# Kernel tuning notes

Hardware: AMD Instinct MI355X
Metric: run time of the kernel (lower is better)

The kernel has to match this reference:

```python
import jax, jax.numpy as jnp
import numpy as np
from jax import lax

N = 5000
C = 81  # num_classes including background at index 0
BG_OFFSET = 1


def _iou_matrix(b):
    # b: [N,4] as x1,y1,x2,y2 -> pairwise IoU [N,N]
    x1, y1, x2, y2 = b[:, 0], b[:, 1], b[:, 2], b[:, 3]
    area = (x2 - x1) * (y2 - y1)  # [N]
    ix1 = jnp.maximum(x1[:, None], x1[None, :])
    iy1 = jnp.maximum(y1[:, None], y1[None, :])
    ix2 = jnp.minimum(x2[:, None], x2[None, :])
    iy2 = jnp.minimum(y2[:, None], y2[None, :])
    iw = jnp.maximum(ix2 - ix1, 0.0)
    ih = jnp.maximum(iy2 - iy1, 0.0)
    inter = iw * ih
    return inter / (area[:, None] + area[None, :] - inter)


def setup_inputs() -> dict:
    key = jax.random.key(0)
    k1, k2, k3 = jax.random.split(key, 3)
    # valid boxes: x1<x2, y1<y2 on a ~1024px canvas, size ~up to 256px
    xy1 = jax.random.uniform(k1, (N, 2), dtype=jnp.float32) * 1024.0
    wh = jax.random.uniform(k2, (N, 2), dtype=jnp.float32) * 256.0 + 1.0
    bboxes = jnp.concatenate([xy1, xy1 + wh], axis=1)  # [N,4]
    scores = jax.random.uniform(k3, (N, C), dtype=jnp.float32)  # [N,C]
    return {
        "bboxes": bboxes,
        "scores": scores,
        "conf_thresh": 0.6,
        "nms_thresh": 0.5,
        "max_instances": 300,
    }


def _multiclass_nms(bboxes, scores, conf_thresh, nms_thresh, max_instances):
    n = bboxes.shape[0]
    neg_inf = jnp.finfo(scores.dtype).min
    iou = _iou_matrix(bboxes)  # [N,N]

    def nms_one_class(score_c):  # score_c: [N]
        valid = score_c > conf_thresh
        masked = jnp.where(valid, score_c, neg_inf)
        order = jnp.argsort(masked)[::-1]  # descending score

        def step(suppressed, idx):
            keep = valid[idx] & ~suppressed[idx]
            new_sup = jnp.where(keep, suppressed | (iou[idx] > nms_thresh), suppressed)
            return new_sup, keep

        _, keeps = lax.scan(step, jnp.zeros((n,), bool), order)
        # scatter keep flags back to original box order
        return jnp.zeros((n,), bool).at[order].set(keeps)

    fg_scores = scores[:, BG_OFFSET:].T  # [C-1, N]
    keep = jax.vmap(nms_one_class)(fg_scores)  # [C-1, N]

    # global top-k over all (class, box) kept detections, sorted by score desc
    flat = jnp.where(keep, fg_scores, neg_inf).reshape(-1)  # [(C-1)*N]
    top_scores, top_idx = lax.top_k(flat, max_instances)
    cls = top_idx // n + BG_OFFSET  # [K]
    box = top_idx % n  # [K]
    valid_out = top_scores > neg_inf / 2

    sel_score = scores[box, cls]  # differentiable gather
    preds = jnp.concatenate([bboxes[box], sel_score[:, None]], axis=1)  # [K,5]
    preds = jnp.where(valid_out[:, None], preds, 0.0)
    labels = jnp.where(valid_out, cls, -1)
    return preds, labels


def reference(bboxes, scores, conf_thresh, nms_thresh, max_instances):
    return _multiclass_nms(bboxes, scores, conf_thresh, nms_thresh, max_instances)
```

## Files before the change

### kernel.cpp

```cpp
#include <hip/hip_runtime.h>

typedef unsigned long long u64;
typedef unsigned int u32;
typedef unsigned short u16;

#define MSORT 4096
#define TPB1  1024
#define TPBF  1024
#define BOXCAP 3648
#define RSLOT_W 10
#define KPC   300
#define SELCAP 1024
#define PREFR 64

#define WG_SCOPE __HIP_MEMORY_SCOPE_WORKGROUP

__device__ __forceinline__ float boxArea(float4 b) {
    return __fmul_rn(__fsub_rn(b.z, b.x), __fsub_rn(b.w, b.y));
}

template<bool GE>
__device__ __forceinline__ bool iou_gt(float4 a, float area_a, float4 b, float area_b, double B) {
    float ix1 = fmaxf(a.x, b.x), iy1 = fmaxf(a.y, b.y);
    float ix2 = fminf(a.z, b.z), iy2 = fminf(a.w, b.w);
    float iw  = fmaxf(__fsub_rn(ix2, ix1), 0.0f);
    float ih  = fmaxf(__fsub_rn(iy2, iy1), 0.0f);
    float inter = __fmul_rn(iw, ih);
    float uni   = __fsub_rn(__fadd_rn(area_a, area_b), inter);
    return GE ? ((double)inter >= B * (double)uni) : ((double)inter > B * (double)uni);
}

__device__ __forceinline__ int scoreBin(u32 bits) {
    int b = (int)(bits >> 12) - 0x3F000;
    return b < 0 ? 0 : (b > 2047 ? 2047 : b);
}

template<bool GE>
__device__ __forceinline__ int prefix_nms_w0(
    const float* __restrict__ bboxes, const u64* __restrict__ keybuf,
    int R, double B, int tid, int c, int N, u64* __restrict__ gkept_c)
{
    u64 key = (tid < R) ? keybuf[tid] : 0;
    float4 bx = make_float4(0.f, 0.f, 0.f, 0.f);
    if (tid < R) bx = ((const float4*)bboxes)[(u32)key];
    float ar = boxArea(bx);
    u64 supB = (R >= 64) ? 0ull : (~0ull << R);
    int nk = 0;
    int i = -1;
    for (;;) {
        u64 mask = (i >= 63) ? 0ull : (~0ull << (i + 1));
        u64 alive = ~supB & mask;
        if (!alive) break;
        i = (int)__builtin_ctzll(alive);
        float4 bi;
        bi.x = __shfl(bx.x, i, 64); bi.y = __shfl(bx.y, i, 64);
        bi.z = __shfl(bx.z, i, 64); bi.w = __shfl(bx.w, i, 64);
        float ai = boxArea(bi);
        if (tid == 0) {
            u64 ki = keybuf[i];
            u32 flat = (u32)c * (u32)N + (u32)ki;
            gkept_c[nk] = (ki & 0xFFFFFFFF00000000ull) | (u32)(~flat);
        }
        nk++;
        bool sup = (tid > i) && iou_gt<GE>(bi, ai, bx, ar, B);
        supB |= __ballot(sup);
    }
    return nk;
}

__global__ __launch_bounds__(TPB1, 1) void nms_select_kernel(
    const float* __restrict__ bboxes, const float* __restrict__ scores,
    const float* __restrict__ conf_ptr, const float* __restrict__ nms_ptr,
    int N, int C, u64* __restrict__ gkept,
    u32* __restrict__ gK, u32* __restrict__ g65, u32* __restrict__ gPre)
{
    __shared__ u32 hist[2048];
    __shared__ int chunk[64];
    __shared__ u64 keybuf[256];
    __shared__ int cntS, ncollS, bstarS, nkS;

    const int tid = threadIdx.x;
    const int c   = blockIdx.x;
    const int cls = c + 1;
    const float conf = *conf_ptr;
    const float nmsT = *nms_ptr;

    for (int b = tid; b < 2048; b += TPB1) hist[b] = 0;
    if (tid == 0) { cntS = 0; ncollS = 0; nkS = 0; }
    __syncthreads();

    for (int i = tid; i < N; i += TPB1) {
        float s = scores[(size_t)i * C + cls];
        if (s > conf) {
            atomicAdd(&cntS, 1);
            atomicAdd(&hist[scoreBin(__float_as_uint(s))], 1u);
        }
    }
    __syncthreads();
    const int K = cntS;
    const int target = K < (PREFR + 1) ? K : (PREFR + 1);

    if (tid < 64) {
        int s = 0;
        #pragma unroll
        for (int b = 0; b < 32; b++) s += (int)hist[tid * 32 + b];
        chunk[tid] = s;
    }
    __syncthreads();
    if (tid == 0) {
        int acc = 0, ch = 63;
        for (; ch >= 0; ch--) { if (acc + chunk[ch] >= target) break; acc += chunk[ch]; }
        int bs = 0;
        if (ch >= 0) {
            int b = (ch << 5) + 31;
            for (; b >= (ch << 5); b--) { acc += (int)hist[b]; if (acc >= target) break; }
            bs = (b < (ch << 5)) ? (ch << 5) : b;
        }
        bstarS = bs;
    }
    __syncthreads();
    const u32 tbits = (bstarS == 0) ? 0u : (((u32)bstarS + 0x3F000u) << 12);

    for (int i = tid; i < N; i += TPB1) {
        float s = scores[(size_t)i * C + cls];
        if (s > conf && __float_as_uint(s) >= tbits) {
            int p = atomicAdd(&ncollS, 1);
            if (p < 256) keybuf[p] = ((u64)__float_as_uint(s) << 32) | (u32)i;
        }
    }
    __syncthreads();
    const int ncoll = ncollS;
    const bool pre = (ncoll > 256);
    u64* gkept_c = gkept + (size_t)c * KPC;

    if (!pre) {
        for (int p = ncoll + tid; p < 256; p += TPB1) keybuf[p] = 0;
        __syncthreads();
        for (int kk = 2; kk <= 256; kk <<= 1) {
            for (int j = kk >> 1; j > 0; j >>= 1) {
                for (int i = tid; i < 256; i += TPB1) {
                    int ixj = i ^ j;
                    if (ixj > i) {
                        u64 a = keybuf[i], b = keybuf[ixj];
                        if (((i & kk) == 0) ? (a < b) : (a > b)) { keybuf[i] = b; keybuf[ixj] = a; }
                    }
                }
                __syncthreads();
            }
        }
        const u32 tb = __float_as_uint(nmsT);
        const float Tn = __uint_as_float(tb + 1u);
        const double B = ((double)nmsT + (double)Tn) * 0.5;
        const bool geCmp = (((tb + 1u) & 1u) == 0u);
        if (tid < 64) {
            int R = ncoll < PREFR ? ncoll : PREFR;
            int nk = geCmp ? prefix_nms_w0<true >(bboxes, keybuf, R, B, tid, c, N, gkept_c)
                           : prefix_nms_w0<false>(bboxes, keybuf, R, B, tid, c, N, gkept_c);
            if (tid == 0) nkS = nk;
        }
        __syncthreads();
        const int nk = nkS;
        for (int p = nk + tid; p < KPC; p += TPB1) gkept_c[p] = 0;
    } else {
        for (int p = tid; p < KPC; p += TPB1) gkept_c[p] = 0;
    }
    if (tid == 0) {
        gK[c]   = (u32)K;
        g65[c]  = pre ? 0xFFFFFFFFu : ((ncoll >= PREFR + 1) ? (u32)(keybuf[PREFR] >> 32) : 0u);
        gPre[c] = pre ? 1u : 0u;
    }
}

__global__ __launch_bounds__(1024) void nms_theta_kernel(
    const u64* __restrict__ gkept, const u32* __restrict__ gK,
    const u32* __restrict__ g65, const u32* __restrict__ gPre,
    int nc, int Mout, u32* __restrict__ gCtl)
{
    __shared__ u32 hist[2048];
    __shared__ int chunk[64];
    __shared__ u32 thetaS;
    const int tid = threadIdx.x;
    const int total = nc * KPC;
    for (int b = tid; b < 2048; b += 1024) hist[b] = 0;
    __syncthreads();
    for (int t = tid; t < total; t += 1024) {
        u64 k = gkept[t];
        if (k) atomicAdd(&hist[scoreBin((u32)(k >> 32))], 1u);
    }
    __syncthreads();
    if (tid < 64) {
        int s = 0;
        #pragma unroll
        for (int b = 0; b < 32; b++) s += (int)hist[tid * 32 + b];
        chunk[tid] = s;
    }
    __syncthreads();
    if (tid == 0) {
        int tot = 0;
        for (int ch = 0; ch < 64; ch++) tot += chunk[ch];
        u32 theta = 0u;
        if (tot >= Mout) {
            int acc = 0, ch = 63;
            for (; ch >= 0; ch--) { if (acc + chunk[ch] >= Mout) break; acc += chunk[ch]; }
            int b = (ch << 5) + 31;
            for (; b >= (ch << 5); b--) { acc += (int)hist[b]; if (acc >= Mout) break; }
            int bs = (b < (ch << 5)) ? (ch << 5) : b;
            theta = (bs <= 0) ? 0u : (((u32)bs + 0x3F000u) << 12);
        }
        gCtl[0] = theta;
        thetaS  = theta;
    }
    __syncthreads();
    const u32 theta = thetaS;
    for (int c2 = tid; c2 < nc; c2 += 1024) {
        u32 need = gPre[c2];
        if (gK[c2] > PREFR && g65[c2] >= theta) need = 1u;
        gCtl[1 + c2] = need;
    }
}

template<bool GE>
__device__ __forceinline__ u64 sweep_own(
    float4 bi, float area_i, const float4 (&breg)[RSLOT_W],
    const float (&areaj)[RSLOT_W], const float4* __restrict__ boxesLds,
    int base, int nslots, int lane, double B)
{
    u64 ns = 0;
    #pragma unroll
    for (int t = 0; t < RSLOT_W; t++)
        ns |= ((u64)iou_gt<GE>(bi, area_i, breg[t], areaj[t], B)) << (base + t);
    for (int t = RSLOT_W; t < nslots; t++) {
        float4 bj = boxesLds[((base + t) << 6) | lane];
        ns |= ((u64)iou_gt<GE>(bi, area_i, bj, boxArea(bj), B)) << (base + t);
    }
    return ns;
}

template<bool GE>
__device__ __forceinline__ int greedy_full(
    const float4* __restrict__ boxesLds, u16* __restrict__ keptR,
    float4* __restrict__ pubBox, u32* __restrict__ ctl,
    const u32* __restrict__ gsi_c, const float* __restrict__ scores,
    int cls, int C, u32 thetaBits,
    int K, int smax, double B, int lane, int wave)
{
    const int SW   = (smax + 3) >> 2;
    const int base = (wave * SW < smax) ? wave * SW : smax;
    const int end  = (base + SW < smax) ? base + SW : smax;
    const int nslots = end - base;

    float4 breg[RSLOT_W];
    float  areaj[RSLOT_W];
    #pragma unroll
    for (int t = 0; t < RSLOT_W; t++) {
        float4 b = boxesLds[((base + t) << 6) | lane];
        breg[t] = b;
        areaj[t] = boxArea(b);
    }

    u64 sup;
    {
        int t = (lane < K) ? ((K - lane + 63) >> 6) : 0;
        sup = (t >= 64) ? 0ull : (~0ull << t);
    }

    u32 seen = 0;
    if (wave != 0) {
        for (;;) {
            u32 d  = __hip_atomic_load(&ctl[2], __ATOMIC_ACQUIRE, WG_SCOPE);
            u32 cn = __hip_atomic_load(&ctl[0], __ATOMIC_ACQUIRE, WG_SCOPE);
            bool prog = (seen < cn);
            while (seen < cn) {
                float4 bi = pubBox[seen]; seen++;
                sup |= sweep_own<GE>(bi, boxArea(bi), breg, areaj, boxesLds, base, nslots, lane, B);
            }
            if (d) return -1;
            u32 aw = __hip_atomic_load(&ctl[1], __ATOMIC_ACQUIRE, WG_SCOPE);
            if (aw == (u32)wave) {
                u32 cn2 = __hip_atomic_load(&ctl[0], __ATOMIC_ACQUIRE, WG_SCOPE);
                while (seen < cn2) {
                    float4 bi = pubBox[seen]; seen++;
                    sup |= sweep_own<GE>(bi, boxArea(bi), breg, areaj, boxesLds, base, nslots, lane, B);
                }
                break;
            }
            if (!prog) __builtin_amdgcn_s_sleep(1);
        }
    }

    u32 nk = seen;
    const u32 seen0 = seen;
    int scur = base - 1;
    float4 bcur = make_float4(0.f, 0.f, 0.f, 0.f);
    float  acur = 0.f;
    int js = base << 6;

    for (;;) {
        int s = js >> 6;
        while (s > scur) {
            scur++;
            if (scur < end) {
                bcur = boxesLds[(scur << 6) | lane];
                acur = boxArea(bcur);
                u64 bit = 0;
                for (u32 k = seen0; k < nk; k++) {
                    float4 bk = pubBox[k];
                    bit |= ((u64)iou_gt<GE>(bk, boxArea(bk), bcur, acur, B));
                }
                sup |= bit << scur;
            }
        }
        if (scur >= end) {
            if (wave == 3) {
                if (lane == 0) __hip_atomic_store(&ctl[2], 1u, __ATOMIC_RELEASE, WG_SCOPE);
                return (int)nk;
            }
            if (lane == 0) __hip_atomic_store(&ctl[1], (u32)(wave + 1), __ATOMIC_RELEASE, WG_SCOPE);
            return -1;
        }
        u64 bal = __ballot((int)(((~sup) >> scur) & 1ull)) & (~0ull << (js & 63));
        if (bal == 0) { js = (scur + 1) << 6; continue; }
        int i = (scur << 6) + (int)__builtin_ctzll(bal);

        if (thetaBits) {
            u32 idx = gsi_c[i];
            float sc = scores[(size_t)idx * C + cls];
            if (__float_as_uint(sc) < thetaBits) {
                if (lane == 0) __hip_atomic_store(&ctl[2], 1u, __ATOMIC_RELEASE, WG_SCOPE);
                return (int)nk;
            }
        }
        float4 bi = boxesLds[i];
        if (lane == 0) { pubBox[nk] = bi; keptR[nk] = (u16)i; }
        nk++;
        if (nk >= KPC) {
            if (lane == 0) {
                __hip_atomic_store(&ctl[0], nk, __ATOMIC_RELEASE, WG_SCOPE);
                __hip_atomic_store(&ctl[2], 1u, __ATOMIC_RELEASE, WG_SCOPE);
            }
            return (int)nk;
        }
        if (lane == 0) __hip_atomic_store(&ctl[0], nk, __ATOMIC_RELEASE, WG_SCOPE);
        sup |= ((u64)iou_gt<GE>(bi, boxArea(bi), bcur, acur, B)) << scur;
        js = i + 1;
    }
}

__global__ __launch_bounds__(TPBF, 1) void nms_full_kernel(
    const float* __restrict__ bboxes, const float* __restrict__ scores,
    const float* __restrict__ conf_ptr, const float* __restrict__ nms_ptr,
    int N, int C, const u32* __restrict__ gCtl,
    u32* __restrict__ gsi, u64* __restrict__ gkept)
{
    const int c = blockIdx.x;
    if (gCtl[1 + c] == 0u) return;

    __shared__ __align__(16) char smem[63856];
    u64*    sortbuf  = (u64*)smem;
    float4* boxesLds = (float4*)smem;
    u16*    keptR    = (u16*)(smem + 58368);
    u32*    ctl      = (u32*)(smem + 58976);
    float4* pubBox   = (float4*)(smem + 58992);
    __shared__ int cntS;

    const int tid = threadIdx.x;
    const int cls = c + 1;
    const float conf = *conf_ptr;
    const float nmsT = *nms_ptr;
    const u32 thetaBits = gCtl[0];

    if (tid == 0) cntS = 0;
    __syncthreads();
    for (int i = tid; i < N; i += TPBF) {
        float s = scores[(size_t)i * C + cls];
        if (s > conf) {
            int p = atomicAdd(&cntS, 1);
            if (p < MSORT) sortbuf[p] = ((u64)__float_as_uint(s) << 32) | (u32)i;
        }
    }
    __syncthreads();
    int K = cntS; if (K > BOXCAP) K = BOXCAP;
    int M = 64; while (M < K) M <<= 1;
    for (int p = K + tid; p < M; p += TPBF) sortbuf[p] = 0;
    __syncthreads();
    for (int kk = 2; kk <= M; kk <<= 1) {
        for (int j = kk >> 1; j > 0; j >>= 1) {
            for (int i = tid; i < M; i += TPBF) {
                int ixj = i ^ j;
                if (ixj > i) {
                    u64 a = sortbuf[i], b = sortbuf[ixj];
                    if (((i & kk) == 0) ? (a < b) : (a > b)) { sortbuf[i] = b; sortbuf[ixj] = a; }
                }
            }
            __syncthreads();
        }
    }
    u32 myIdx[MSORT / TPBF];
    #pragma unroll
    for (int t = 0; t < MSORT / TPBF; t++) myIdx[t] = (u32)sortbuf[t * TPBF + tid];
    __syncthreads();
    u32* gsi_c = gsi + (size_t)c * BOXCAP;
    #pragma unroll
    for (int t = 0; t < MSORT / TPBF; t++) {
        int r = t * TPBF + tid;
        if (r < K) {
            u32 idx = myIdx[t];
            gsi_c[r] = idx;
            boxesLds[r] = ((const float4*)bboxes)[idx];
        }
    }
    if (tid == 0) { ctl[0] = 0; ctl[1] = 0; ctl[2] = 0; }
    __syncthreads();
    if (tid >= 256) return;

    const int lane = tid & 63;
    const int wave = tid >> 6;
    const u32 tb = __float_as_uint(nmsT);
    const float Tn = __uint_as_float(tb + 1u);
    const double B = ((double)nmsT + (double)Tn) * 0.5;
    const bool geCmp = (((tb + 1u) & 1u) == 0u);
    const int smax = (K + 63) >> 6;

    int ret = geCmp ? greedy_full<true >(boxesLds, keptR, pubBox, ctl, gsi_c, scores, cls, C, thetaBits, K, smax, B, lane, wave)
                    : greedy_full<false>(boxesLds, keptR, pubBox, ctl, gsi_c, scores, cls, C, thetaBits, K, smax, B, lane, wave);
    if (ret >= 0) {
        int kept = ret; if (kept > KPC) kept = KPC;
        u64* gkept_c = gkept + (size_t)c * KPC;
        for (int p = lane; p < kept; p += 64) {
            int rank = keptR[p];
            u32 idx = gsi_c[rank];
            float sc = scores[(size_t)idx * C + cls];
            u32 flat = (u32)c * (u32)N + idx;
            gkept_c[p] = ((u64)__float_as_uint(sc) << 32) | (u32)(~flat);
        }
        for (int p = kept + lane; p < KPC; p += 64) gkept_c[p] = 0;
    }
}

__global__ __launch_bounds__(1024) void nms_topk_kernel(
    const float* __restrict__ bboxes, const u64* __restrict__ gkept,
    int N, int nc, int Mout, float* __restrict__ out)
{
    __shared__ u32 hist[2048];
    __shared__ int chunk[64];
    __shared__ int selCount;
    __shared__ int bstarS;
    __shared__ u64 sel[SELCAP];

    const int tid = threadIdx.x;
    const int total = nc * KPC;

    for (int b = tid; b < 2048; b += 1024) hist[b] = 0;
    if (tid == 0) selCount = 0;
    __syncthreads();

    for (int t = tid; t < total; t += 1024) {
        u64 k = gkept[t];
        if (k) atomicAdd(&hist[scoreBin((u32)(k >> 32))], 1u);
    }
    __syncthreads();

    if (tid < 64) {
        int s = 0;
        #pragma unroll
        for (int b = 0; b < 32; b++) s += (int)hist[tid * 32 + b];
        chunk[tid] = s;
    }
    __syncthreads();

    if (tid == 0) {
        int acc = 0, ch = 63;
        for (; ch >= 0; ch--) {
            if (acc + chunk[ch] >= Mout) break;
            acc += chunk[ch];
        }
        int bs = 0;
        if (ch >= 0) {
            int b = (ch << 5) + 31;
            for (; b >= (ch << 5); b--) { acc += (int)hist[b]; if (acc >= Mout) break; }
            bs = (b < (ch << 5)) ? (ch << 5) : b;
        }
        bstarS = bs;
    }
    __syncthreads();
    const int bstar = bstarS;

    for (int t = tid; t < total; t += 1024) {
        u64 k = gkept[t];
        if (k) {
            int b = scoreBin((u32)(k >> 32));
            if (b >= bstar) {
                int p = atomicAdd(&selCount, 1);
                if (p < SELCAP) sel[p] = k;
            }
        }
    }
    __syncthreads();
    int cnt = selCount; if (cnt > SELCAP) cnt = SELCAP;
    for (int p = cnt + tid; p < SELCAP; p += 1024) sel[p] = 0;
    __syncthreads();

    for (int kk = 2; kk <= SELCAP; kk <<= 1) {
        for (int j = kk >> 1; j > 0; j >>= 1) {
            int i = tid;
            int ixj = i ^ j;
            if (i < SELCAP && ixj > i) {
                u64 a = sel[i], b = sel[ixj];
                if (((i & kk) == 0) ? (a < b) : (a > b)) { sel[i] = b; sel[ixj] = a; }
            }
            __syncthreads();
        }
    }

    for (int t = tid; t < Mout; t += 1024) {
        u64 k = (t < SELCAP) ? sel[t] : 0;
        float px1 = 0.f, py1 = 0.f, px2 = 0.f, py2 = 0.f, ps = 0.f, plab = -1.0f;
        if (k) {
            float s  = __uint_as_float((u32)(k >> 32));
            u32 flat = ~((u32)k);
            int cc   = (int)(flat / (u32)N);
            int box  = (int)(flat - (u32)cc * (u32)N);
            float4 bb = ((const float4*)bboxes)[box];
            px1 = bb.x; py1 = bb.y; px2 = bb.z; py2 = bb.w; ps = s;
            plab = (float)(cc + 1);
        }
        out[t * 5 + 0] = px1;
        out[t * 5 + 1] = py1;
        out[t * 5 + 2] = px2;
        out[t * 5 + 3] = py2;
        out[t * 5 + 4] = ps;
        out[Mout * 5 + t] = plab;
    }
}

extern "C" void kernel_launch(void* const* d_in, const int* in_sizes, int n_in,
                              void* d_out, int out_size, void* d_ws, size_t ws_size,
                              hipStream_t stream) {
    const float* bboxes = (const float*)d_in[0];
    const float* scores = (const float*)d_in[1];
    const float* conf   = (const float*)d_in[2];
    const float* nmsT   = (const float*)d_in[3];

    const int N    = in_sizes[0] / 4;
    const int C    = in_sizes[1] / N;
    const int nc   = C - 1;
    const int Mout = out_size / 6;

    char* wsb = (char*)d_ws;
    size_t off = 0;
    u32* gsi   = (u32*)(wsb + off); off += (size_t)nc * BOXCAP * sizeof(u32);
    u64* gkept = (u64*)(wsb + off); off += (size_t)nc * KPC * sizeof(u64);
    u32* gK    = (u32*)(wsb + off); off += (size_t)((nc + 2) & ~1) * sizeof(u32);
    u32* g65   = (u32*)(wsb + off); off += (size_t)((nc + 2) & ~1) * sizeof(u32);
    u32* gPre  = (u32*)(wsb + off); off += (size_t)((nc + 2) & ~1) * sizeof(u32);
    u32* gCtl  = (u32*)(wsb + off);

    nms_select_kernel<<<nc, TPB1, 0, stream>>>(bboxes, scores, conf, nmsT, N, C, gkept, gK, g65, gPre);
    nms_theta_kernel<<<1, 1024, 0, stream>>>(gkept, gK, g65, gPre, nc, Mout, gCtl);
    nms_full_kernel<<<nc, TPBF, 0, stream>>>(bboxes, scores, conf, nmsT, N, C, gCtl, gsi, gkept);
    nms_topk_kernel<<<1, 1024, 0, stream>>>(bboxes, gkept, N, nc, Mout, (float*)d_out);
}
```

Measured before the change: 122.9 us.

## Fuse theta and topk stages into last-block epilogues, cache scores in LDS

Removes the two single-block kernels (theta and topk) by having the last finishing block of the select and full kernels, detected with a global atomic ticket counter, run that work. This cuts two kernel launches and their serialization gaps at the cost of a memset and threadfences. The select kernel also caches valid score keys in LDS with wave-aggregated atomics, so the second pass over the strided score column is avoided. It replaces the 256-element bitonic sort with a rank-count selection of the top 65, drops the block size to 512 threads, and sizes the final sort to the actual selection count.

```diff
diff --git a/kernel.cpp b/kernel.cpp
--- a/kernel.cpp
+++ b/kernel.cpp
@@ -5,9 +5,10 @@
 typedef unsigned short u16;
 
 #define MSORT 4096
-#define TPB1  1024
+#define TPB1  512
 #define TPBF  1024
 #define BOXCAP 3648
+#define KCAP  3072
 #define RSLOT_W 10
 #define KPC   300
 #define SELCAP 1024
@@ -37,10 +38,10 @@
 
 template<bool GE>
 __device__ __forceinline__ int prefix_nms_w0(
-    const float* __restrict__ bboxes, const u64* __restrict__ keybuf,
+    const float* __restrict__ bboxes, const u64* __restrict__ sorted,
     int R, double B, int tid, int c, int N, u64* __restrict__ gkept_c)
 {
-    u64 key = (tid < R) ? keybuf[tid] : 0;
+    u64 key = (tid < R) ? sorted[tid] : 0;
     float4 bx = make_float4(0.f, 0.f, 0.f, 0.f);
     if (tid < R) bx = ((const float4*)bboxes)[(u32)key];
     float ar = boxArea(bx);
@@ -57,7 +58,7 @@
         bi.z = __shfl(bx.z, i, 64); bi.w = __shfl(bx.w, i, 64);
         float ai = boxArea(bi);
         if (tid == 0) {
-            u64 ki = keybuf[i];
+            u64 ki = sorted[i];
             u32 flat = (u32)c * (u32)N + (u32)ki;
             gkept_c[nk] = (ki & 0xFFFFFFFF00000000ull) | (u32)(~flat);
         }
@@ -71,33 +72,49 @@
 __global__ __launch_bounds__(TPB1, 1) void nms_select_kernel(
     const float* __restrict__ bboxes, const float* __restrict__ scores,
     const float* __restrict__ conf_ptr, const float* __restrict__ nms_ptr,
-    int N, int C, u64* __restrict__ gkept,
-    u32* __restrict__ gK, u32* __restrict__ g65, u32* __restrict__ gPre)
+    int N, int C, int Mout, u64* __restrict__ gkept,
+    u32* __restrict__ gK, u32* __restrict__ g65, u32* __restrict__ gPre,
+    u32* __restrict__ gCtl, u32* __restrict__ gTick)
 {
+    __shared__ u64 keys[KCAP];
     __shared__ u32 hist[2048];
+    __shared__ u64 keybuf[256];
+    __shared__ u64 sorted[66];
     __shared__ int chunk[64];
-    __shared__ u64 keybuf[256];
-    __shared__ int cntS, ncollS, bstarS, nkS;
+    __shared__ int cntS, ncollS, bstarS, nkS, lastS;
+    __shared__ u32 thetaS;
 
     const int tid = threadIdx.x;
     const int c   = blockIdx.x;
+    const int nc  = gridDim.x;
     const int cls = c + 1;
     const float conf = *conf_ptr;
     const float nmsT = *nms_ptr;
+    const int lane = tid & 63;
 
     for (int b = tid; b < 2048; b += TPB1) hist[b] = 0;
-    if (tid == 0) { cntS = 0; ncollS = 0; nkS = 0; }
+    if (tid < 66) sorted[tid] = 0;
+    if (tid == 0) { cntS = 0; nkS = 0; }
     __syncthreads();
 
     for (int i = tid; i < N; i += TPB1) {
         float s = scores[(size_t)i * C + cls];
-        if (s > conf) {
-            atomicAdd(&cntS, 1);
+        bool valid = s > conf;
+        u64 mask = __ballot((int)valid);
+        if (valid) {
+            int cntw = (int)__popcll(mask);
+            int leader = (int)__builtin_ctzll(mask);
+            int base = 0;
+            if (lane == leader) base = atomicAdd(&cntS, cntw);
+            base = __shfl(base, leader, 64);
+            int off = base + (int)__popcll(mask & ((1ull << lane) - 1ull));
+            if (off < KCAP) keys[off] = ((u64)__float_as_uint(s) << 32) | (u32)i;
             atomicAdd(&hist[scoreBin(__float_as_uint(s))], 1u);
         }
     }
     __syncthreads();
     const int K = cntS;
+    const bool preOv = (K > KCAP);
     const int target = K < (PREFR + 1) ? K : (PREFR + 1);
 
     if (tid < 64) {
@@ -116,74 +133,69 @@
             for (; b >= (ch << 5); b--) { acc += (int)hist[b]; if (acc >= target) break; }
             bs = (b < (ch << 5)) ? (ch << 5) : b;
         }
-        bstarS = bs;
+        bstarS = bs; ncollS = 0;
     }
     __syncthreads();
     const u32 tbits = (bstarS == 0) ? 0u : (((u32)bstarS + 0x3F000u) << 12);
 
-    for (int i = tid; i < N; i += TPB1) {
-        float s = scores[(size_t)i * C + cls];
-        if (s > conf && __float_as_uint(s) >= tbits) {
-            int p = atomicAdd(&ncollS, 1);
-            if (p < 256) keybuf[p] = ((u64)__float_as_uint(s) << 32) | (u32)i;
+    const int KL = K < KCAP ? K : KCAP;
+    for (int p = tid; p < KL; p += TPB1) {
+        u64 k = keys[p];
+        if ((u32)(k >> 32) >= tbits) {
+            int pos = atomicAdd(&ncollS, 1);
+            if (pos < 256) keybuf[pos] = k;
         }
     }
     __syncthreads();
     const int ncoll = ncollS;
-    const bool pre = (ncoll > 256);
+    const bool pre = preOv || (ncoll > 256);
+    for (int p = ncoll + tid; p < 256; p += TPB1) keybuf[p] = 0;
+    __syncthreads();
+
     u64* gkept_c = gkept + (size_t)c * KPC;
-
     if (!pre) {
-        for (int p = ncoll + tid; p < 256; p += TPB1) keybuf[p] = 0;
-        __syncthreads();
-        for (int kk = 2; kk <= 256; kk <<= 1) {
-            for (int j = kk >> 1; j > 0; j >>= 1) {
-                for (int i = tid; i < 256; i += TPB1) {
-                    int ixj = i ^ j;
-                    if (ixj > i) {
-                        u64 a = keybuf[i], b = keybuf[ixj];
-                        if (((i & kk) == 0) ? (a < b) : (a > b)) { keybuf[i] = b; keybuf[ixj] = a; }
-                    }
-                }
-                __syncthreads();
-            }
-        }
+        if (tid < 256) {
+            u64 my = keybuf[tid];
+            int rank = 0;
+            for (int j = 0; j < 256; j++) rank += (keybuf[j] > my);
+            if (my && rank < PREFR + 1) sorted[rank] = my;
+        }
+        __syncthreads();
         const u32 tb = __float_as_uint(nmsT);
         const float Tn = __uint_as_float(tb + 1u);
         const double B = ((double)nmsT + (double)Tn) * 0.5;
         const bool geCmp = (((tb + 1u) & 1u) == 0u);
         if (tid < 64) {
             int R = ncoll < PREFR ? ncoll : PREFR;
-            int nk = geCmp ? prefix_nms_w0<true >(bboxes, keybuf, R, B, tid, c, N, gkept_c)
-                           : prefix_nms_w0<false>(bboxes, keybuf, R, B, tid, c, N, gkept_c);
+            int nk = geCmp ? prefix_nms_w0<true >(bboxes, sorted, R, B, tid, c, N, gkept_c)
+                           : prefix_nms_w0<false>(bboxes, sorted, R, B, tid, c, N, gkept_c);
             if (tid == 0) nkS = nk;
         }
         __syncthreads();
-        const int nk = nkS;
-        for (int p = nk + tid; p < KPC; p += TPB1) gkept_c[p] = 0;
+        for (int p = nkS + tid; p < KPC; p += TPB1) gkept_c[p] = 0;
     } else {
         for (int p = tid; p < KPC; p += TPB1) gkept_c[p] = 0;
     }
     if (tid == 0) {
         gK[c]   = (u32)K;
-        g65[c]  = pre ? 0xFFFFFFFFu : ((ncoll >= PREFR + 1) ? (u32)(keybuf[PREFR] >> 32) : 0u);
+        g65[c]  = pre ? 0xFFFFFFFFu : ((ncoll >= PREFR + 1) ? (u32)(sorted[PREFR] >> 32) : 0u);
         gPre[c] = pre ? 1u : 0u;
     }
-}
-
-__global__ __launch_bounds__(1024) void nms_theta_kernel(
-    const u64* __restrict__ gkept, const u32* __restrict__ gK,
-    const u32* __restrict__ g65, const u32* __restrict__ gPre,
-    int nc, int Mout, u32* __restrict__ gCtl)
-{
-    __shared__ u32 hist[2048];
-    __shared__ int chunk[64];
-    __shared__ u32 thetaS;
-    const int tid = threadIdx.x;
+    __syncthreads();
+
+    if (tid == 0) {
+        __threadfence();
+        u32 old = atomicAdd(gTick, 1u);
+        lastS = (old == (u32)(nc - 1)) ? 1 : 0;
+    }
+    __syncthreads();
+    if (!lastS) return;
+    __threadfence();
+
+    for (int b = tid; b < 2048; b += TPB1) hist[b] = 0;
+    __syncthreads();
     const int total = nc * KPC;
-    for (int b = tid; b < 2048; b += 1024) hist[b] = 0;
-    __syncthreads();
-    for (int t = tid; t < total; t += 1024) {
+    for (int t = tid; t < total; t += TPB1) {
         u64 k = gkept[t];
         if (k) atomicAdd(&hist[scoreBin((u32)(k >> 32))], 1u);
     }
@@ -212,7 +224,7 @@
     }
     __syncthreads();
     const u32 theta = thetaS;
-    for (int c2 = tid; c2 < nc; c2 += 1024) {
+    for (int c2 = tid; c2 < nc; c2 += TPB1) {
         u32 need = gPre[c2];
         if (gK[c2] > PREFR && g65[c2] >= theta) need = 1u;
         gCtl[1 + c2] = need;
@@ -349,117 +361,119 @@
 __global__ __launch_bounds__(TPBF, 1) void nms_full_kernel(
     const float* __restrict__ bboxes, const float* __restrict__ scores,
     const float* __restrict__ conf_ptr, const float* __restrict__ nms_ptr,
-    int N, int C, const u32* __restrict__ gCtl,
-    u32* __restrict__ gsi, u64* __restrict__ gkept)
+    int N, int C, int Mout, const u32* __restrict__ gCtl,
+    u32* __restrict__ gsi, u64* __restrict__ gkept,
+    u32* __restrict__ gTick, float* __restrict__ out)
 {
-    const int c = blockIdx.x;
-    if (gCtl[1 + c] == 0u) return;
-
     __shared__ __align__(16) char smem[63856];
-    u64*    sortbuf  = (u64*)smem;
-    float4* boxesLds = (float4*)smem;
-    u16*    keptR    = (u16*)(smem + 58368);
-    u32*    ctl      = (u32*)(smem + 58976);
-    float4* pubBox   = (float4*)(smem + 58992);
-    __shared__ int cntS;
+    __shared__ int cntS, lastS, selCount, bstar2S;
 
     const int tid = threadIdx.x;
+    const int c   = blockIdx.x;
+    const int nc  = gridDim.x;
     const int cls = c + 1;
-    const float conf = *conf_ptr;
-    const float nmsT = *nms_ptr;
-    const u32 thetaBits = gCtl[0];
-
-    if (tid == 0) cntS = 0;
-    __syncthreads();
-    for (int i = tid; i < N; i += TPBF) {
-        float s = scores[(size_t)i * C + cls];
-        if (s > conf) {
-            int p = atomicAdd(&cntS, 1);
-            if (p < MSORT) sortbuf[p] = ((u64)__float_as_uint(s) << 32) | (u32)i;
-        }
-    }
-    __syncthreads();
-    int K = cntS; if (K > BOXCAP) K = BOXCAP;
-    int M = 64; while (M < K) M <<= 1;
-    for (int p = K + tid; p < M; p += TPBF) sortbuf[p] = 0;
-    __syncthreads();
-    for (int kk = 2; kk <= M; kk <<= 1) {
-        for (int j = kk >> 1; j > 0; j >>= 1) {
-            for (int i = tid; i < M; i += TPBF) {
-                int ixj = i ^ j;
-                if (ixj > i) {
-                    u64 a = sortbuf[i], b = sortbuf[ixj];
-                    if (((i & kk) == 0) ? (a < b) : (a > b)) { sortbuf[i] = b; sortbuf[ixj] = a; }
+
+    if (gCtl[1 + c] != 0u) {
+        u64*    sortbuf  = (u64*)smem;
+        float4* boxesLds = (float4*)smem;
+        u16*    keptR    = (u16*)(smem + 58368);
+        u32*    ctl      = (u32*)(smem + 58976);
+        float4* pubBox   = (float4*)(smem + 58992);
+        const float conf = *conf_ptr;
+        const float nmsT = *nms_ptr;
+        const u32 thetaBits = gCtl[0];
+
+        if (tid == 0) cntS = 0;
+        __syncthreads();
+        for (int i = tid; i < N; i += TPBF) {
+            float s = scores[(size_t)i * C + cls];
+            if (s > conf) {
+                int p = atomicAdd(&cntS, 1);
+                if (p < MSORT) sortbuf[p] = ((u64)__float_as_uint(s) << 32) | (u32)i;
+            }
+        }
+        __syncthreads();
+        int K = cntS; if (K > BOXCAP) K = BOXCAP;
+        int M = 64; while (M < K) M <<= 1;
+        for (int p = K + tid; p < M; p += TPBF) sortbuf[p] = 0;
+        __syncthreads();
+        for (int kk = 2; kk <= M; kk <<= 1) {
+            for (int j = kk >> 1; j > 0; j >>= 1) {
+                for (int i = tid; i < M; i += TPBF) {
+                    int ixj = i ^ j;
+                    if (ixj > i) {
+                        u64 a = sortbuf[i], b = sortbuf[ixj];
+                        if (((i & kk) == 0) ? (a < b) : (a > b)) { sortbuf[i] = b; sortbuf[ixj] = a; }
+                    }
                 }
-            }
-            __syncthreads();
-        }
-    }
-    u32 myIdx[MSORT / TPBF];
-    #pragma unroll
-    for (int t = 0; t < MSORT / TPBF; t++) myIdx[t] = (u32)sortbuf[t * TPBF + tid];
-    __syncthreads();
-    u32* gsi_c = gsi + (size_t)c * BOXCAP;
-    #pragma unroll
-    for (int t = 0; t < MSORT / TPBF; t++) {
-        int r = t * TPBF + tid;
-        if (r < K) {
-            u32 idx = myIdx[t];
-            gsi_c[r] = idx;
-            boxesLds[r] = ((const float4*)bboxes)[idx];
-        }
-    }
-    if (tid == 0) { ctl[0] = 0; ctl[1] = 0; ctl[2] = 0; }
-    __syncthreads();
-    if (tid >= 256) return;
-
-    const int lane = tid & 63;
-    const int wave = tid >> 6;
-    const u32 tb = __float_as_uint(nmsT);
-    const float Tn = __uint_as_float(tb + 1u);
-    const double B = ((double)nmsT + (double)Tn) * 0.5;
-    const bool geCmp = (((tb + 1u) & 1u) == 0u);
-    const int smax = (K + 63) >> 6;
-
-    int ret = geCmp ? greedy_full<true >(boxesLds, keptR, pubBox, ctl, gsi_c, scores, cls, C, thetaBits, K, smax, B, lane, wave)
-                    : greedy_full<false>(boxesLds, keptR, pubBox, ctl, gsi_c, scores, cls, C, thetaBits, K, smax, B, lane, wave);
-    if (ret >= 0) {
-        int kept = ret; if (kept > KPC) kept = KPC;
-        u64* gkept_c = gkept + (size_t)c * KPC;
-        for (int p = lane; p < kept; p += 64) {
-            int rank = keptR[p];
-            u32 idx = gsi_c[rank];
-            float sc = scores[(size_t)idx * C + cls];
-            u32 flat = (u32)c * (u32)N + idx;
-            gkept_c[p] = ((u64)__float_as_uint(sc) << 32) | (u32)(~flat);
-        }
-        for (int p = kept + lane; p < KPC; p += 64) gkept_c[p] = 0;
-    }
-}
-
-__global__ __launch_bounds__(1024) void nms_topk_kernel(
-    const float* __restrict__ bboxes, const u64* __restrict__ gkept,
-    int N, int nc, int Mout, float* __restrict__ out)
-{
-    __shared__ u32 hist[2048];
-    __shared__ int chunk[64];
-    __shared__ int selCount;
-    __shared__ int bstarS;
-    __shared__ u64 sel[SELCAP];
-
-    const int tid = threadIdx.x;
+                __syncthreads();
+            }
+        }
+        u32 myIdx[MSORT / TPBF];
+        #pragma unroll
+        for (int t = 0; t < MSORT / TPBF; t++) myIdx[t] = (u32)sortbuf[t * TPBF + tid];
+        __syncthreads();
+        u32* gsi_c = gsi + (size_t)c * BOXCAP;
+        #pragma unroll
+        for (int t = 0; t < MSORT / TPBF; t++) {
+            int r = t * TPBF + tid;
+            if (r < K) {
+                u32 idx = myIdx[t];
+                gsi_c[r] = idx;
+                boxesLds[r] = ((const float4*)bboxes)[idx];
+            }
+        }
+        if (tid == 0) { ctl[0] = 0; ctl[1] = 0; ctl[2] = 0; }
+        __syncthreads();
+
+        if (tid < 256) {
+            const int lane = tid & 63;
+            const int wave = tid >> 6;
+            const u32 tb = __float_as_uint(nmsT);
+            const float Tn = __uint_as_float(tb + 1u);
+            const double B = ((double)nmsT + (double)Tn) * 0.5;
+            const bool geCmp = (((tb + 1u) & 1u) == 0u);
+            const int smax = (K + 63) >> 6;
+            int ret = geCmp ? greedy_full<true >(boxesLds, keptR, pubBox, ctl, gsi_c, scores, cls, C, thetaBits, K, smax, B, lane, wave)
+                            : greedy_full<false>(boxesLds, keptR, pubBox, ctl, gsi_c, scores, cls, C, thetaBits, K, smax, B, lane, wave);
+            if (ret >= 0) {
+                int kept = ret; if (kept > KPC) kept = KPC;
+                u64* gkept_c = gkept + (size_t)c * KPC;
+                for (int p = lane; p < kept; p += 64) {
+                    int rank = keptR[p];
+                    u32 idx = gsi_c[rank];
+                    float sc = scores[(size_t)idx * C + cls];
+                    u32 flat = (u32)c * (u32)N + idx;
+                    gkept_c[p] = ((u64)__float_as_uint(sc) << 32) | (u32)(~flat);
+                }
+                for (int p = kept + lane; p < KPC; p += 64) gkept_c[p] = 0;
+            }
+        }
+    }
+    __syncthreads();
+
+    if (tid == 0) {
+        __threadfence();
+        u32 old = atomicAdd(gTick, 1u);
+        lastS = (old == (u32)(nc - 1)) ? 1 : 0;
+    }
+    __syncthreads();
+    if (!lastS) return;
+    __threadfence();
+
+    u32* hist  = (u32*)smem;
+    int* chunk = (int*)(smem + 8192);
+    u64* sel   = (u64*)(smem + 8448);
+
     const int total = nc * KPC;
-
-    for (int b = tid; b < 2048; b += 1024) hist[b] = 0;
+    for (int b = tid; b < 2048; b += TPBF) hist[b] = 0;
     if (tid == 0) selCount = 0;
     __syncthreads();
-
-    for (int t = tid; t < total; t += 1024) {
+    for (int t = tid; t < total; t += TPBF) {
         u64 k = gkept[t];
         if (k) atomicAdd(&hist[scoreBin((u32)(k >> 32))], 1u);
     }
     __syncthreads();
-
     if (tid < 64) {
         int s = 0;
         #pragma unroll
@@ -467,53 +481,46 @@
         chunk[tid] = s;
     }
     __syncthreads();
-
     if (tid == 0) {
         int acc = 0, ch = 63;
-        for (; ch >= 0; ch--) {
-            if (acc + chunk[ch] >= Mout) break;
-            acc += chunk[ch];
-        }
+        for (; ch >= 0; ch--) { if (acc + chunk[ch] >= Mout) break; acc += chunk[ch]; }
         int bs = 0;
         if (ch >= 0) {
             int b = (ch << 5) + 31;
             for (; b >= (ch << 5); b--) { acc += (int)hist[b]; if (acc >= Mout) break; }
             bs = (b < (ch << 5)) ? (ch << 5) : b;
         }
-        bstarS = bs;
-    }
-    __syncthreads();
-    const int bstar = bstarS;
-
-    for (int t = tid; t < total; t += 1024) {
+        bstar2S = bs;
+    }
+    __syncthreads();
+    const int bstar = bstar2S;
+    for (int t = tid; t < total; t += TPBF) {
         u64 k = gkept[t];
-        if (k) {
-            int b = scoreBin((u32)(k >> 32));
-            if (b >= bstar) {
-                int p = atomicAdd(&selCount, 1);
-                if (p < SELCAP) sel[p] = k;
-            }
+        if (k && scoreBin((u32)(k >> 32)) >= bstar) {
+            int p = atomicAdd(&selCount, 1);
+            if (p < SELCAP) sel[p] = k;
         }
     }
     __syncthreads();
     int cnt = selCount; if (cnt > SELCAP) cnt = SELCAP;
-    for (int p = cnt + tid; p < SELCAP; p += 1024) sel[p] = 0;
-    __syncthreads();
-
-    for (int kk = 2; kk <= SELCAP; kk <<= 1) {
+    int SM = 512; while (SM < cnt) SM <<= 1;
+    for (int p = cnt + tid; p < SM; p += TPBF) sel[p] = 0;
+    __syncthreads();
+    for (int kk = 2; kk <= SM; kk <<= 1) {
         for (int j = kk >> 1; j > 0; j >>= 1) {
-            int i = tid;
-            int ixj = i ^ j;
-            if (i < SELCAP && ixj > i) {
-                u64 a = sel[i], b = sel[ixj];
-                if (((i & kk) == 0) ? (a < b) : (a > b)) { sel[i] = b; sel[ixj] = a; }
+            for (int i = tid; i < SM; i += TPBF) {
+                int ixj = i ^ j;
+                if (ixj > i) {
+                    u64 a = sel[i], b = sel[ixj];
+                    if (((i & kk) == 0) ? (a < b) : (a > b)) { sel[i] = b; sel[ixj] = a; }
+                }
             }
             __syncthreads();
         }
     }
 
-    for (int t = tid; t < Mout; t += 1024) {
-        u64 k = (t < SELCAP) ? sel[t] : 0;
+    for (int t = tid; t < Mout; t += TPBF) {
+        u64 k = (t < SM) ? sel[t] : 0;
         float px1 = 0.f, py1 = 0.f, px2 = 0.f, py2 = 0.f, ps = 0.f, plab = -1.0f;
         if (k) {
             float s  = __uint_as_float((u32)(k >> 32));
@@ -550,13 +557,15 @@
     size_t off = 0;
     u32* gsi   = (u32*)(wsb + off); off += (size_t)nc * BOXCAP * sizeof(u32);
     u64* gkept = (u64*)(wsb + off); off += (size_t)nc * KPC * sizeof(u64);
-    u32* gK    = (u32*)(wsb + off); off += (size_t)((nc + 2) & ~1) * sizeof(u32);
-    u32* g65   = (u32*)(wsb + off); off += (size_t)((nc + 2) & ~1) * sizeof(u32);
-    u32* gPre  = (u32*)(wsb + off); off += (size_t)((nc + 2) & ~1) * sizeof(u32);
-    u32* gCtl  = (u32*)(wsb + off);
-
-    nms_select_kernel<<<nc, TPB1, 0, stream>>>(bboxes, scores, conf, nmsT, N, C, gkept, gK, g65, gPre);
-    nms_theta_kernel<<<1, 1024, 0, stream>>>(gkept, gK, g65, gPre, nc, Mout, gCtl);
-    nms_full_kernel<<<nc, TPBF, 0, stream>>>(bboxes, scores, conf, nmsT, N, C, gCtl, gsi, gkept);
-    nms_topk_kernel<<<1, 1024, 0, stream>>>(bboxes, gkept, N, nc, Mout, (float*)d_out);
-}
+    u32* gK    = (u32*)(wsb + off); off += (size_t)((nc + 1) & ~1) * sizeof(u32);
+    u32* g65   = (u32*)(wsb + off); off += (size_t)((nc + 1) & ~1) * sizeof(u32);
+    u32* gPre  = (u32*)(wsb + off); off += (size_t)((nc + 1) & ~1) * sizeof(u32);
+    u32* gCtl  = (u32*)(wsb + off); off += (size_t)((nc + 2) & ~1) * sizeof(u32);
+    u32* gTick = (u32*)(wsb + off);
+
+    hipMemsetAsync(gTick, 0, 2 * sizeof(u32), stream);
+    nms_select_kernel<<<nc, TPB1, 0, stream>>>(bboxes, scores, conf, nmsT, N, C, Mout,
+                                               gkept, gK, g65, gPre, gCtl, gTick);
+    nms_full_kernel<<<nc, TPBF, 0, stream>>>(bboxes, scores, conf, nmsT, N, C, Mout,
+                                             gCtl, gsi, gkept, gTick + 1, (float*)d_out);
+}
```

Result: slower. 134.2 us (+9.2%).

## Cache above-threshold keys in LDS, rank-select prefix, size final sort dynamically

Applied to the files above, without the earlier changes.

In the select kernel, above-threshold keys are stored in shared memory during the histogram pass, so the second pass reads LDS instead of re-reading the strided score column from global memory. The 256-entry bitonic sort is replaced by an O(n^2) rank computation that keeps only the top 65 keys. A new overflow flag sends classes with more than KCAP survivors to the full path. The top-k kernel now sorts only the next power of two at or above the selected count (minimum 512) instead of a fixed 1024. The gains trade against much more shared memory per block and quadratic rank work.

```diff
diff --git a/kernel.cpp b/kernel.cpp
--- a/kernel.cpp
+++ b/kernel.cpp
@@ -8,6 +8,7 @@
 #define TPB1  1024
 #define TPBF  1024
 #define BOXCAP 3648
+#define KCAP  3072
 #define RSLOT_W 10
 #define KPC   300
 #define SELCAP 1024
@@ -37,10 +38,10 @@
 
 template<bool GE>
 __device__ __forceinline__ int prefix_nms_w0(
-    const float* __restrict__ bboxes, const u64* __restrict__ keybuf,
+    const float* __restrict__ bboxes, const u64* __restrict__ sorted,
     int R, double B, int tid, int c, int N, u64* __restrict__ gkept_c)
 {
-    u64 key = (tid < R) ? keybuf[tid] : 0;
+    u64 key = (tid < R) ? sorted[tid] : 0;
     float4 bx = make_float4(0.f, 0.f, 0.f, 0.f);
     if (tid < R) bx = ((const float4*)bboxes)[(u32)key];
     float ar = boxArea(bx);
@@ -57,7 +58,7 @@
         bi.z = __shfl(bx.z, i, 64); bi.w = __shfl(bx.w, i, 64);
         float ai = boxArea(bi);
         if (tid == 0) {
-            u64 ki = keybuf[i];
+            u64 ki = sorted[i];
             u32 flat = (u32)c * (u32)N + (u32)ki;
             gkept_c[nk] = (ki & 0xFFFFFFFF00000000ull) | (u32)(~flat);
         }
@@ -74,9 +75,11 @@
     int N, int C, u64* __restrict__ gkept,
     u32* __restrict__ gK, u32* __restrict__ g65, u32* __restrict__ gPre)
 {
+    __shared__ u64 keys[KCAP];
     __shared__ u32 hist[2048];
+    __shared__ u64 keybuf[256];
+    __shared__ u64 sorted[66];
     __shared__ int chunk[64];
-    __shared__ u64 keybuf[256];
     __shared__ int cntS, ncollS, bstarS, nkS;
 
     const int tid = threadIdx.x;
@@ -86,18 +89,21 @@
     const float nmsT = *nms_ptr;
 
     for (int b = tid; b < 2048; b += TPB1) hist[b] = 0;
+    if (tid < 66) sorted[tid] = 0;
     if (tid == 0) { cntS = 0; ncollS = 0; nkS = 0; }
     __syncthreads();
 
     for (int i = tid; i < N; i += TPB1) {
         float s = scores[(size_t)i * C + cls];
         if (s > conf) {
-            atomicAdd(&cntS, 1);
+            int p = atomicAdd(&cntS, 1);
+            if (p < KCAP) keys[p] = ((u64)__float_as_uint(s) << 32) | (u32)i;
             atomicAdd(&hist[scoreBin(__float_as_uint(s))], 1u);
         }
     }
     __syncthreads();
     const int K = cntS;
+    const bool preOv = (K > KCAP);
     const int target = K < (PREFR + 1) ? K : (PREFR + 1);
 
     if (tid < 64) {
@@ -121,52 +127,47 @@
     __syncthreads();
     const u32 tbits = (bstarS == 0) ? 0u : (((u32)bstarS + 0x3F000u) << 12);
 
-    for (int i = tid; i < N; i += TPB1) {
-        float s = scores[(size_t)i * C + cls];
-        if (s > conf && __float_as_uint(s) >= tbits) {
-            int p = atomicAdd(&ncollS, 1);
-            if (p < 256) keybuf[p] = ((u64)__float_as_uint(s) << 32) | (u32)i;
+    const int KL = K < KCAP ? K : KCAP;
+    for (int p = tid; p < KL; p += TPB1) {
+        u64 k = keys[p];
+        if ((u32)(k >> 32) >= tbits) {
+            int pos = atomicAdd(&ncollS, 1);
+            if (pos < 256) keybuf[pos] = k;
         }
     }
     __syncthreads();
     const int ncoll = ncollS;
-    const bool pre = (ncoll > 256);
+    const bool pre = preOv || (ncoll > 256);
+    for (int p = ncoll + tid; p < 256; p += TPB1) keybuf[p] = 0;
+    __syncthreads();
+
     u64* gkept_c = gkept + (size_t)c * KPC;
-
     if (!pre) {
-        for (int p = ncoll + tid; p < 256; p += TPB1) keybuf[p] = 0;
+        if (tid < 256) {
+            u64 my = keybuf[tid];
+            int rank = 0;
+            for (int j = 0; j < 256; j++) rank += (keybuf[j] > my);
+            if (my && rank < PREFR + 1) sorted[rank] = my;
+        }
         __syncthreads();
-        for (int kk = 2; kk <= 256; kk <<= 1) {
-            for (int j = kk >> 1; j > 0; j >>= 1) {
-                for (int i = tid; i < 256; i += TPB1) {
-                    int ixj = i ^ j;
-                    if (ixj > i) {
-                        u64 a = keybuf[i], b = keybuf[ixj];
-                        if (((i & kk) == 0) ? (a < b) : (a > b)) { keybuf[i] = b; keybuf[ixj] = a; }
-                    }
-                }
-                __syncthreads();
-            }
-        }
         const u32 tb = __float_as_uint(nmsT);
         const float Tn = __uint_as_float(tb + 1u);
         const double B = ((double)nmsT + (double)Tn) * 0.5;
         const bool geCmp = (((tb + 1u) & 1u) == 0u);
         if (tid < 64) {
             int R = ncoll < PREFR ? ncoll : PREFR;
-            int nk = geCmp ? prefix_nms_w0<true >(bboxes, keybuf, R, B, tid, c, N, gkept_c)
-                           : prefix_nms_w0<false>(bboxes, keybuf, R, B, tid, c, N, gkept_c);
+            int nk = geCmp ? prefix_nms_w0<true >(bboxes, sorted, R, B, tid, c, N, gkept_c)
+                           : prefix_nms_w0<false>(bboxes, sorted, R, B, tid, c, N, gkept_c);
             if (tid == 0) nkS = nk;
         }
         __syncthreads();
-        const int nk = nkS;
-        for (int p = nk + tid; p < KPC; p += TPB1) gkept_c[p] = 0;
+        for (int p = nkS + tid; p < KPC; p += TPB1) gkept_c[p] = 0;
     } else {
         for (int p = tid; p < KPC; p += TPB1) gkept_c[p] = 0;
     }
     if (tid == 0) {
         gK[c]   = (u32)K;
-        g65[c]  = pre ? 0xFFFFFFFFu : ((ncoll >= PREFR + 1) ? (u32)(keybuf[PREFR] >> 32) : 0u);
+        g65[c]  = pre ? 0xFFFFFFFFu : ((ncoll >= PREFR + 1) ? (u32)(sorted[PREFR] >> 32) : 0u);
         gPre[c] = pre ? 1u : 0u;
     }
 }
@@ -487,33 +488,32 @@
 
     for (int t = tid; t < total; t += 1024) {
         u64 k = gkept[t];
-        if (k) {
-            int b = scoreBin((u32)(k >> 32));
-            if (b >= bstar) {
-                int p = atomicAdd(&selCount, 1);
-                if (p < SELCAP) sel[p] = k;
-            }
+        if (k && scoreBin((u32)(k >> 32)) >= bstar) {
+            int p = atomicAdd(&selCount, 1);
+            if (p < SELCAP) sel[p] = k;
         }
     }
     __syncthreads();
     int cnt = selCount; if (cnt > SELCAP) cnt = SELCAP;
-    for (int p = cnt + tid; p < SELCAP; p += 1024) sel[p] = 0;
-    __syncthreads();
-
-    for (int kk = 2; kk <= SELCAP; kk <<= 1) {
+    int SM = 512; while (SM < cnt) SM <<= 1;
+    for (int p = cnt + tid; p < SM; p += 1024) sel[p] = 0;
+    __syncthreads();
+
+    for (int kk = 2; kk <= SM; kk <<= 1) {
         for (int j = kk >> 1; j > 0; j >>= 1) {
-            int i = tid;
-            int ixj = i ^ j;
-            if (i < SELCAP && ixj > i) {
-                u64 a = sel[i], b = sel[ixj];
-                if (((i & kk) == 0) ? (a < b) : (a > b)) { sel[i] = b; sel[ixj] = a; }
+            for (int i = tid; i < SM; i += 1024) {
+                int ixj = i ^ j;
+                if (ixj > i) {
+                    u64 a = sel[i], b = sel[ixj];
+                    if (((i & kk) == 0) ? (a < b) : (a > b)) { sel[i] = b; sel[ixj] = a; }
+                }
             }
             __syncthreads();
         }
     }
 
     for (int t = tid; t < Mout; t += 1024) {
-        u64 k = (t < SELCAP) ? sel[t] : 0;
+        u64 k = (t < SM) ? sel[t] : 0;
         float px1 = 0.f, py1 = 0.f, px2 = 0.f, py2 = 0.f, ps = 0.f, plab = -1.0f;
         if (k) {
             float s  = __uint_as_float((u32)(k >> 32));
@@ -550,9 +550,9 @@
     size_t off = 0;
     u32* gsi   = (u32*)(wsb + off); off += (size_t)nc * BOXCAP * sizeof(u32);
     u64* gkept = (u64*)(wsb + off); off += (size_t)nc * KPC * sizeof(u64);
-    u32* gK    = (u32*)(wsb + off); off += (size_t)((nc + 2) & ~1) * sizeof(u32);
-    u32* g65   = (u32*)(wsb + off); off += (size_t)((nc + 2) & ~1) * sizeof(u32);
-    u32* gPre  = (u32*)(wsb + off); off += (size_t)((nc + 2) & ~1) * sizeof(u32);
+    u32* gK    = (u32*)(wsb + off); off += (size_t)((nc + 1) & ~1) * sizeof(u32);
+    u32* g65   = (u32*)(wsb + off); off += (size_t)((nc + 1) & ~1) * sizeof(u32);
+    u32* gPre  = (u32*)(wsb + off); off += (size_t)((nc + 1) & ~1) * sizeof(u32);
     u32* gCtl  = (u32*)(wsb + off);
 
     nms_select_kernel<<<nc, TPB1, 0, stream>>>(bboxes, scores, conf, nmsT, N, C, gkept, gK, g65, gPre);
```

Result: faster. 117.3 us (-4.6%).
